# Optimization experiments

Measured on AMD Instinct MI355X. Metric: run time of the kernel, lower is better.

The kernel has to match this reference:

```python
import jax, jax.numpy as jnp
import numpy as np

B, S, D, V = 16384, 20, 128, 12  # batch, max_seq_len, embed_dim, num_embeddings
EPS = 1e-5


def _rmsnorm_ax1(x, w):
    # RMSNorm over axis=1 of [B, S, D], learnable scale of shape [S]
    ms = jnp.mean(x * x, axis=1, keepdims=True)
    return x * jax.lax.rsqrt(ms + EPS) * w[None, :, None]


def _dwconv(x, w, b, dil):
    # depthwise conv1d: x [B, S, D], w [S, 1, K], groups=S, 'same' padding
    y = jax.lax.conv_general_dilated(
        x, w, window_strides=(1,), padding=[(dil, dil)],
        rhs_dilation=(dil,), dimension_numbers=('NCH', 'OIH', 'NCH'),
        feature_group_count=x.shape[1])
    return y + b[None, :, None]


def setup_inputs() -> dict:
    key = jax.random.key(0)
    ks = jax.random.split(key, 14)
    sc = 0.05
    return {
        'tokens': jax.random.randint(ks[0], (B, S), 0, V, dtype=jnp.int32),
        'number_log': jax.random.normal(ks[1], (B,), dtype=jnp.float32),
        'emb': jax.random.normal(ks[2], (V, D), dtype=jnp.float32) * sc,
        'pre_w': jnp.ones((S,), dtype=jnp.float32),
        'w0': jax.random.normal(ks[3], (S, 1, 3), dtype=jnp.float32) * sc,
        'b0': jax.random.normal(ks[4], (S,), dtype=jnp.float32) * sc,
        'w1': jax.random.normal(ks[5], (S, 1, 3), dtype=jnp.float32) * sc,
        'b1': jax.random.normal(ks[6], (S,), dtype=jnp.float32) * sc,
        'w2': jax.random.normal(ks[7], (S, 1, 3), dtype=jnp.float32) * sc,
        'b2': jax.random.normal(ks[8], (S,), dtype=jnp.float32) * sc,
        'gate_w': jax.random.normal(ks[9], (S, S), dtype=jnp.float32) * sc,
        'gate_b': jax.random.normal(ks[10], (S,), dtype=jnp.float32) * sc,
        'post_w': jnp.ones((S,), dtype=jnp.float32),
        'logit_w': jax.random.normal(ks[11], (1, S, 1), dtype=jnp.float32) * sc,
    }


def reference(tokens, number_log, emb, pre_w, w0, b0, w1, b1, w2, b2,
              gate_w, gate_b, post_w, logit_w):
    x = emb[tokens]                       # [B, S, D] embedding lookup
    x_norm = _rmsnorm_ax1(x, pre_w)       # pre RMSNorm over seq axis
    x_d = (_dwconv(x_norm, w0, b0, 1)
           + _dwconv(x_norm, w1, b1, 2)
           + _dwconv(x_norm, w2, b2, 4))  # multi-dilation depthwise branches
    # gate: Linear(S,S)+SiLU applied along axis 1 (torch transposes to [B,D,S])
    g = jnp.einsum('bsl,ts->btl', x_norm, gate_w) + gate_b[None, :, None]
    g = jax.nn.silu(g)
    x_d = _rmsnorm_ax1(x_d * g, post_w)
    # final pointwise conv1d S->1, no bias
    out = jnp.einsum('bsl,os->bol', x + x_d, logit_w[:, :, 0])  # [B, 1, D]
    return out
```

## Files before the change

kernel.cpp:

```cpp
#include <hip/hip_runtime.h>
#include <stdint.h>

#define BB 16384
#define SS 20
#define DD 128
#define EPSV 1e-5f


typedef __fp16 half2_t __attribute__((ext_vector_type(2)));

#define BPERMU(addr, v) ((uint32_t)__builtin_amdgcn_ds_bpermute((addr), (int)(v)))

static __device__ __forceinline__ uint32_t pk16(float a, float b) {
    return __builtin_bit_cast(uint32_t, __builtin_amdgcn_cvt_pkrtz(a, b));
}
static __device__ __forceinline__ half2_t h2(uint32_t u) {
    return __builtin_bit_cast(half2_t, u);
}

__global__ void pack_w_kernel(const float* __restrict__ gate_w,
                              const float* __restrict__ w0, const float* __restrict__ b0,
                              const float* __restrict__ w1, const float* __restrict__ b1,
                              const float* __restrict__ w2, const float* __restrict__ b2,
                              uint32_t*    __restrict__ ws) {
    const int i = threadIdx.x;
    if (i < SS * SS) {
        const float v = gate_w[i];
        ws[i] = pk16(v, v);
    }
    if (i < SS) {
        const float wa0 = w0[i*3+0], wam = w0[i*3+1], wa2 = w0[i*3+2];
        const float wb0 = w1[i*3+0], wbm = w1[i*3+1], wb2 = w1[i*3+2];
        const float wc0 = w2[i*3+0], wcm = w2[i*3+1], wc2 = w2[i*3+2];
        const float cw   = wam + wbm + wcm;
        const float bias = b0[i] + b1[i] + b2[i];
        uint32_t* o = ws + SS * SS + i * 8;
        o[0] = pk16(wc0, wc0);  o[1] = pk16(wb0, wb0);
        o[2] = pk16(wa0, wa0);  o[3] = pk16(cw,  cw);
        o[4] = pk16(wa2, wa2);  o[5] = pk16(wb2, wb2);
        o[6] = pk16(wc2, wc2);  o[7] = pk16(bias, bias);
    }
}

__global__ __launch_bounds__(256) void fused_mdt_kernel(
    const int*      __restrict__ tokens,
    const float*    __restrict__ emb,
    const float*    __restrict__ pre_w,
    const uint32_t* __restrict__ wpk,
    const float*    __restrict__ gate_b,
    const float*    __restrict__ post_w,
    const float*    __restrict__ logit_w,
    float*          __restrict__ out)
{
    const int tid  = threadIdx.x;
    const int lane = tid & 63;
    const int b    = __builtin_amdgcn_readfirstlane(blockIdx.x * 4 + (tid >> 6));
    const int d0   = lane << 1;

    const bool mL1 = (lane == 0);
    const bool mL2 = (lane <  2);
    const bool mR1 = (lane == 63);
    const bool mR2 = (lane >= 62);
    const int aL2 = (lane - 2) << 2;
    const int aL1 = (lane - 1) << 2;
    const int aR1 = (lane + 1) << 2;
    const int aR2 = (lane + 2) << 2;

    const int* tb = tokens + b * SS;

    float ms0 = 0.f, ms1 = 0.f, a10 = 0.f, a11 = 0.f;
    #pragma unroll
    for (int s = 0; s < SS; ++s) {
        const float2 v = *reinterpret_cast<const float2*>(emb + tb[s] * DD + d0);
        ms0 = fmaf(v.x, v.x, ms0);
        ms1 = fmaf(v.y, v.y, ms1);
        const float lw = logit_w[s];
        a10 = fmaf(v.x, lw, a10);
        a11 = fmaf(v.y, lw, a11);
    }
    const float r0 = rsqrtf(ms0 * (1.f/SS) + EPSV);
    const float r1 = rsqrtf(ms1 * (1.f/SS) + EPSV);

    __builtin_amdgcn_sched_barrier(0);

    uint32_t X[SS];
    #pragma unroll
    for (int s = 0; s < SS; ++s) {
        const float2 v = *reinterpret_cast<const float2*>(emb + tb[s] * DD + d0);
        const float pw = pre_w[s];
        X[s] = pk16(v.x * (r0 * pw), v.y * (r1 * pw));
    }

    __builtin_amdgcn_sched_barrier(0);

    float m20 = 0.f, m21 = 0.f, ac0 = 0.f, ac1 = 0.f;
    #pragma unroll
    for (int t = 0; t < SS; ++t) {
        uint32_t L2u = BPERMU(aL2, X[t]);
        uint32_t L1u = BPERMU(aL1, X[t]);
        uint32_t R1u = BPERMU(aR1, X[t]);
        uint32_t R2u = BPERMU(aR2, X[t]);
        L2u = mL2 ? 0u : L2u;
        L1u = mL1 ? 0u : L1u;
        R1u = mR1 ? 0u : R1u;
        R2u = mR2 ? 0u : R2u;
        const uint32_t Dm1 = __builtin_amdgcn_alignbit(X[t], L1u, 16);
        const uint32_t Dp1 = __builtin_amdgcn_alignbit(R1u, X[t], 16);

        const uint32_t* cw8 = wpk + SS * SS + t * 8;
        half2_t xd = h2(cw8[7]);
        xd += h2(cw8[0]) * h2(L2u);
        xd += h2(cw8[1]) * h2(L1u);
        xd += h2(cw8[2]) * h2(Dm1);
        xd += h2(cw8[3]) * h2(X[t]);
        xd += h2(cw8[4]) * h2(Dp1);
        xd += h2(cw8[5]) * h2(R1u);
        xd += h2(cw8[6]) * h2(R2u);

        half2_t ga = h2(0u), gb = h2(0u);
        #pragma unroll
        for (int q = 0; q < SS / 2; ++q) {
            ga += h2(wpk[t * SS + 2*q    ]) * h2(X[2*q    ]);
            gb += h2(wpk[t * SS + 2*q + 1]) * h2(X[2*q + 1]);
        }
        const half2_t gp = ga + gb;
        const float gbv = gate_b[t];
        const float g0 = (float)gp[0] + gbv;
        const float g1 = (float)gp[1] + gbv;
        const float xd0 = (float)xd[0];
        const float xd1 = (float)xd[1];

        const float pl = post_w[t] * logit_w[t];
        const float h0 = xd0 * (g0 * __builtin_amdgcn_rcpf(1.f + __expf(-g0)));
        const float h1 = xd1 * (g1 * __builtin_amdgcn_rcpf(1.f + __expf(-g1)));
        m20 = fmaf(h0, h0, m20);
        m21 = fmaf(h1, h1, m21);
        ac0 = fmaf(h0, pl, ac0);
        ac1 = fmaf(h1, pl, ac1);
    }

    const float q0 = rsqrtf(m20 * (1.f/SS) + EPSV);
    const float q1 = rsqrtf(m21 * (1.f/SS) + EPSV);

    float2 res;
    res.x = a10 + q0 * ac0;
    res.y = a11 + q1 * ac1;
    *reinterpret_cast<float2*>(out + b * DD + d0) = res;
}

extern "C" void kernel_launch(void* const* d_in, const int* in_sizes, int n_in,
                              void* d_out, int out_size, void* d_ws, size_t ws_size,
                              hipStream_t stream) {
    const int*   tokens  = (const int*)  d_in[0];
    const float* emb     = (const float*)d_in[2];
    const float* pre_w   = (const float*)d_in[3];
    const float* w0      = (const float*)d_in[4];
    const float* b0      = (const float*)d_in[5];
    const float* w1      = (const float*)d_in[6];
    const float* b1      = (const float*)d_in[7];
    const float* w2      = (const float*)d_in[8];
    const float* b2      = (const float*)d_in[9];
    const float* gate_w  = (const float*)d_in[10];
    const float* gate_b  = (const float*)d_in[11];
    const float* post_w  = (const float*)d_in[12];
    const float* logit_w = (const float*)d_in[13];
    float*       out     = (float*)d_out;
    uint32_t*    ws      = (uint32_t*)d_ws;

    hipLaunchKernelGGL(pack_w_kernel, dim3(1), dim3(512), 0, stream,
                       gate_w, w0, b0, w1, b1, w2, b2, ws);

    dim3 grid(BB / 4);
    dim3 block(256);
    hipLaunchKernelGGL(fused_mdt_kernel, grid, block, 0, stream,
                       tokens, emb, pre_w, (const uint32_t*)ws,
                       gate_b, post_w, logit_w, out);
}
```

Before: 52.31 us.

## Process four channels per lane with half-wave rows and vectorized loads

Each lane now handles four embedding channels instead of two, so a 32-lane half-wave covers one batch row and each wave processes two rows. Embedding loads become float4, tokens are read as int4, and the gate weights are reused across two packed channel pairs. Cross-lane shuffles per row drop from four to four per two packed registers, which halves the shuffle count per channel. In exchange, register pressure per lane roughly doubles, which could lower occupancy, and the grid is halved.

```diff
diff --git a/kernel.cpp b/kernel.cpp
--- a/kernel.cpp
+++ b/kernel.cpp
@@ -54,98 +54,132 @@
 {
     const int tid  = threadIdx.x;
     const int lane = tid & 63;
-    const int b    = __builtin_amdgcn_readfirstlane(blockIdx.x * 4 + (tid >> 6));
-    const int d0   = lane << 1;
-
-    const bool mL1 = (lane == 0);
-    const bool mL2 = (lane <  2);
-    const bool mR1 = (lane == 63);
-    const bool mR2 = (lane >= 62);
-    const int aL2 = (lane - 2) << 2;
-    const int aL1 = (lane - 1) << 2;
-    const int aR1 = (lane + 1) << 2;
-    const int aR2 = (lane + 2) << 2;
-
-    const int* tb = tokens + b * SS;
-
-    float ms0 = 0.f, ms1 = 0.f, a10 = 0.f, a11 = 0.f;
+    const int il   = lane & 31;
+    const int b    = blockIdx.x * 8 + (tid >> 5);
+    const int d0   = il << 2;
+
+    const bool mL = (il == 0);
+    const bool mR = (il == 31);
+    const int  la = (lane - 1) << 2;
+    const int  ra = (lane + 1) << 2;
+
+    const int4* t4 = reinterpret_cast<const int4*>(tokens + b * SS);
+
+    float ms0=0.f, ms1=0.f, ms2=0.f, ms3=0.f;
+    float a10=0.f, a11=0.f, a12=0.f, a13=0.f;
     #pragma unroll
-    for (int s = 0; s < SS; ++s) {
-        const float2 v = *reinterpret_cast<const float2*>(emb + tb[s] * DD + d0);
-        ms0 = fmaf(v.x, v.x, ms0);
-        ms1 = fmaf(v.y, v.y, ms1);
-        const float lw = logit_w[s];
-        a10 = fmaf(v.x, lw, a10);
-        a11 = fmaf(v.y, lw, a11);
+    for (int i = 0; i < 5; ++i) {
+        const int4 tv = t4[i];
+        const int tg[4] = {tv.x, tv.y, tv.z, tv.w};
+        #pragma unroll
+        for (int j = 0; j < 4; ++j) {
+            const int s = 4*i + j;
+            const float4 v = *reinterpret_cast<const float4*>(emb + tg[j] * DD + d0);
+            ms0 = fmaf(v.x, v.x, ms0); ms1 = fmaf(v.y, v.y, ms1);
+            ms2 = fmaf(v.z, v.z, ms2); ms3 = fmaf(v.w, v.w, ms3);
+            const float lw = logit_w[s];
+            a10 = fmaf(v.x, lw, a10); a11 = fmaf(v.y, lw, a11);
+            a12 = fmaf(v.z, lw, a12); a13 = fmaf(v.w, lw, a13);
+        }
     }
     const float r0 = rsqrtf(ms0 * (1.f/SS) + EPSV);
     const float r1 = rsqrtf(ms1 * (1.f/SS) + EPSV);
+    const float r2 = rsqrtf(ms2 * (1.f/SS) + EPSV);
+    const float r3 = rsqrtf(ms3 * (1.f/SS) + EPSV);
 
     __builtin_amdgcn_sched_barrier(0);
 
-    uint32_t X[SS];
+    uint32_t X0[SS], X1[SS];
     #pragma unroll
-    for (int s = 0; s < SS; ++s) {
-        const float2 v = *reinterpret_cast<const float2*>(emb + tb[s] * DD + d0);
-        const float pw = pre_w[s];
-        X[s] = pk16(v.x * (r0 * pw), v.y * (r1 * pw));
+    for (int i = 0; i < 5; ++i) {
+        const int4 tv = t4[i];
+        const int tg[4] = {tv.x, tv.y, tv.z, tv.w};
+        #pragma unroll
+        for (int j = 0; j < 4; ++j) {
+            const int s = 4*i + j;
+            const float4 v = *reinterpret_cast<const float4*>(emb + tg[j] * DD + d0);
+            const float pw = pre_w[s];
+            X0[s] = pk16(v.x * (r0 * pw), v.y * (r1 * pw));
+            X1[s] = pk16(v.z * (r2 * pw), v.w * (r3 * pw));
+        }
     }
 
     __builtin_amdgcn_sched_barrier(0);
 
-    float m20 = 0.f, m21 = 0.f, ac0 = 0.f, ac1 = 0.f;
+    float m20=0.f, m21=0.f, m22=0.f, m23=0.f;
+    float ac0=0.f, ac1=0.f, ac2=0.f, ac3=0.f;
     #pragma unroll
     for (int t = 0; t < SS; ++t) {
-        uint32_t L2u = BPERMU(aL2, X[t]);
-        uint32_t L1u = BPERMU(aL1, X[t]);
-        uint32_t R1u = BPERMU(aR1, X[t]);
-        uint32_t R2u = BPERMU(aR2, X[t]);
-        L2u = mL2 ? 0u : L2u;
-        L1u = mL1 ? 0u : L1u;
-        R1u = mR1 ? 0u : R1u;
-        R2u = mR2 ? 0u : R2u;
-        const uint32_t Dm1 = __builtin_amdgcn_alignbit(X[t], L1u, 16);
-        const uint32_t Dp1 = __builtin_amdgcn_alignbit(R1u, X[t], 16);
+        uint32_t LX0 = BPERMU(la, X0[t]);
+        uint32_t LX1 = BPERMU(la, X1[t]);
+        uint32_t RX0 = BPERMU(ra, X0[t]);
+        uint32_t RX1 = BPERMU(ra, X1[t]);
+        LX0 = mL ? 0u : LX0;  LX1 = mL ? 0u : LX1;
+        RX0 = mR ? 0u : RX0;  RX1 = mR ? 0u : RX1;
+        const uint32_t Dm1 = __builtin_amdgcn_alignbit(X0[t], LX1, 16);
+        const uint32_t Dc  = __builtin_amdgcn_alignbit(X1[t], X0[t], 16);
+        const uint32_t Dp1 = __builtin_amdgcn_alignbit(RX0, X1[t], 16);
 
         const uint32_t* cw8 = wpk + SS * SS + t * 8;
-        half2_t xd = h2(cw8[7]);
-        xd += h2(cw8[0]) * h2(L2u);
-        xd += h2(cw8[1]) * h2(L1u);
-        xd += h2(cw8[2]) * h2(Dm1);
-        xd += h2(cw8[3]) * h2(X[t]);
-        xd += h2(cw8[4]) * h2(Dp1);
-        xd += h2(cw8[5]) * h2(R1u);
-        xd += h2(cw8[6]) * h2(R2u);
-
-        half2_t ga = h2(0u), gb = h2(0u);
+        half2_t xdA = h2(cw8[7]);
+        xdA += h2(cw8[0]) * h2(LX0);
+        xdA += h2(cw8[1]) * h2(LX1);
+        xdA += h2(cw8[2]) * h2(Dm1);
+        xdA += h2(cw8[3]) * h2(X0[t]);
+        xdA += h2(cw8[4]) * h2(Dc);
+        xdA += h2(cw8[5]) * h2(X1[t]);
+        xdA += h2(cw8[6]) * h2(RX0);
+        half2_t xdB = h2(cw8[7]);
+        xdB += h2(cw8[0]) * h2(LX1);
+        xdB += h2(cw8[1]) * h2(X0[t]);
+        xdB += h2(cw8[2]) * h2(Dc);
+        xdB += h2(cw8[3]) * h2(X1[t]);
+        xdB += h2(cw8[4]) * h2(Dp1);
+        xdB += h2(cw8[5]) * h2(RX0);
+        xdB += h2(cw8[6]) * h2(RX1);
+
+        half2_t gaA = h2(0u), gbA = h2(0u), gaB = h2(0u), gbB = h2(0u);
         #pragma unroll
         for (int q = 0; q < SS / 2; ++q) {
-            ga += h2(wpk[t * SS + 2*q    ]) * h2(X[2*q    ]);
-            gb += h2(wpk[t * SS + 2*q + 1]) * h2(X[2*q + 1]);
+            const half2_t hw0 = h2(wpk[t * SS + 2*q    ]);
+            const half2_t hw1 = h2(wpk[t * SS + 2*q + 1]);
+            gaA += hw0 * h2(X0[2*q    ]);
+            gbA += hw1 * h2(X0[2*q + 1]);
+            gaB += hw0 * h2(X1[2*q    ]);
+            gbB += hw1 * h2(X1[2*q + 1]);
         }
-        const half2_t gp = ga + gb;
+        const half2_t gpA = gaA + gbA;
+        const half2_t gpB = gaB + gbB;
         const float gbv = gate_b[t];
-        const float g0 = (float)gp[0] + gbv;
-        const float g1 = (float)gp[1] + gbv;
-        const float xd0 = (float)xd[0];
-        const float xd1 = (float)xd[1];
+        const float g0 = (float)gpA[0] + gbv;
+        const float g1 = (float)gpA[1] + gbv;
+        const float g2 = (float)gpB[0] + gbv;
+        const float g3 = (float)gpB[1] + gbv;
+        const float xd0 = (float)xdA[0], xd1 = (float)xdA[1];
+        const float xd2 = (float)xdB[0], xd3 = (float)xdB[1];
 
         const float pl = post_w[t] * logit_w[t];
         const float h0 = xd0 * (g0 * __builtin_amdgcn_rcpf(1.f + __expf(-g0)));
         const float h1 = xd1 * (g1 * __builtin_amdgcn_rcpf(1.f + __expf(-g1)));
-        m20 = fmaf(h0, h0, m20);
-        m21 = fmaf(h1, h1, m21);
-        ac0 = fmaf(h0, pl, ac0);
-        ac1 = fmaf(h1, pl, ac1);
+        const float h2v = xd2 * (g2 * __builtin_amdgcn_rcpf(1.f + __expf(-g2)));
+        const float h3 = xd3 * (g3 * __builtin_amdgcn_rcpf(1.f + __expf(-g3)));
+        m20 = fmaf(h0, h0, m20); m21 = fmaf(h1, h1, m21);
+        m22 = fmaf(h2v, h2v, m22); m23 = fmaf(h3, h3, m23);
+        ac0 = fmaf(h0, pl, ac0); ac1 = fmaf(h1, pl, ac1);
+        ac2 = fmaf(h2v, pl, ac2); ac3 = fmaf(h3, pl, ac3);
     }
 
     const float q0 = rsqrtf(m20 * (1.f/SS) + EPSV);
     const float q1 = rsqrtf(m21 * (1.f/SS) + EPSV);
-
-    float2 res;
+    const float q2 = rsqrtf(m22 * (1.f/SS) + EPSV);
+    const float q3 = rsqrtf(m23 * (1.f/SS) + EPSV);
+
+    float4 res;
     res.x = a10 + q0 * ac0;
     res.y = a11 + q1 * ac1;
-    *reinterpret_cast<float2*>(out + b * DD + d0) = res;
+    res.z = a12 + q2 * ac2;
+    res.w = a13 + q3 * ac3;
+    *reinterpret_cast<float4*>(out + b * DD + d0) = res;
 }
 
 extern "C" void kernel_launch(void* const* d_in, const int* in_sizes, int n_in,
@@ -170,7 +204,7 @@
     hipLaunchKernelGGL(pack_w_kernel, dim3(1), dim3(512), 0, stream,
                        gate_w, w0, b0, w1, b1, w2, b2, ws);
 
-    dim3 grid(BB / 4);
+    dim3 grid(BB / 8);
     dim3 block(256);
     hipLaunchKernelGGL(fused_mdt_kernel, grid, block, 0, stream,
                        tokens, emb, pre_w, (const uint32_t*)ws,
```

Result: no change. 52.09 us (-0.4%).
